# Kernel optimization log

Measured on AMD Instinct MI355X. Metric: run time of the kernel, lower is better.

The kernel has to match this reference:

```python
import jax, jax.numpy as jnp
import numpy as np

BIT_SIZE = 128  # N: bitstream length (init arg bit_size)


def setup_inputs() -> dict:
    key = jax.random.key(0)
    k1, k2 = jax.random.split(key)
    # Input bitstreams: (batch, D, N) of 0/1 bits
    inputs = jax.random.randint(k1, (64, 1024, BIT_SIZE), 0, 2, dtype=jnp.int32)
    # Learned kernel probabilities: (num_outputs, D) in [0, 1]
    kernel = jax.random.uniform(k2, (512, 1024), dtype=jnp.float32)
    return {"inputs": inputs, "kernel": kernel}


def _generate_weight_bitstreams(kernel, N):
    # Faithful vectorization of bitstream_generator_exact applied per weight:
    # exactly round(p*N) ones placed at uniformly random positions.
    p = jnp.clip(kernel, 0.0, 1.0)
    n_bits = jnp.round(p * N)  # (O, D)
    u = jax.random.uniform(jax.random.key(42), p.shape + (N,))
    # rank of each position in a random permutation
    ranks = jnp.argsort(jnp.argsort(u, axis=-1), axis=-1)  # (O, D, N)
    return (ranks < n_bits[..., None]).astype(jnp.int32)   # (O, D, N) 0/1


def reference(inputs, kernel):
    N = BIT_SIZE
    wbits = _generate_weight_bitstreams(kernel, N)  # (O, D, N)
    # AND of 0/1 bits == product; popcount-accumulate over input dim D.
    # out[b, o, t] = sum_d (w[o, d, t] & x[b, d, t])
    counts = jnp.einsum('odn,bdn->bon', wbits, inputs)  # (B, O, N) int32
    # Stochastic-computing value estimate: normalize by bitstream length.
    return counts.astype(jnp.float32) / N
```

## Files before the change

kernel.cpp:

```cpp
#include <hip/hip_runtime.h>
#include <stdint.h>

#define B_ 64
#define D_ 1024
#define O_ 512
#define N_ 128

__device__ __forceinline__ uint32_t rotl32(uint32_t x, uint32_t d) {
  return __builtin_amdgcn_alignbit(x, x, 32u - d);
}

__device__ __forceinline__ void threefry2x32(uint32_t c0, uint32_t c1,
                                             uint32_t& r0, uint32_t& r1) {
  const uint32_t ks0 = 0u;
  const uint32_t ks1 = 42u;
  const uint32_t ks2 = 0u ^ 42u ^ 0x1BD11BDAu;
  uint32_t x0 = c0 + ks0;
  uint32_t x1 = c1 + ks1;
#define RND(R) { x0 += x1; x1 = rotl32(x1, R); x1 ^= x0; }
  RND(13) RND(15) RND(26) RND(6)
  x0 += ks1; x1 += ks2 + 1u;
  RND(17) RND(29) RND(16) RND(24)
  x0 += ks2; x1 += ks0 + 2u;
  RND(13) RND(15) RND(26) RND(6)
  x0 += ks0; x1 += ks1 + 3u;
  RND(17) RND(29) RND(16) RND(24)
  x0 += ks1; x1 += ks2 + 4u;
  RND(13) RND(15) RND(26) RND(6)
  x0 += ks2; x1 += ks0 + 5u;
#undef RND
  r0 = x0; r1 = x1;
}

__device__ __forceinline__ uint32_t rand_bits(uint32_t i) {
  uint32_t a, b;
  threefry2x32(0u, i, a, b);
  return a ^ b;
}

__global__ void pack_x(const int* __restrict__ x, uint32_t* __restrict__ xp) {
  const int t   = threadIdx.x;
  const int idx = blockIdx.x;
  const int b   = idx >> 5;
  const int g   = (idx >> 2) & 7;
  const int e   = idx & 3;
  const int* src = x + ((b * D_) + (g * 128 + e * 32)) * N_ + t;
  uint32_t w = 0;
#pragma unroll
  for (int j = 0; j < 32; ++j)
    w |= (uint32_t)(src[j * N_] & 1) << j;
  xp[(((b * 8) + g) * N_ + t) * 4 + e] = w;
}

__global__ void gen_weights(const float* __restrict__ kern, uint4* __restrict__ wtmp) {
  const int lane = threadIdx.x & 63;
  const int wave = threadIdx.x >> 6;
  const int row0 = blockIdx.x * 32 + wave * 8;
  const uint32_t lane2 = (uint32_t)lane + 64u;
  const uint32_t KMASK = 0xFFFFFF80u;
  const uint32_t base_i = (uint32_t)row0 * 128u + (uint32_t)lane;

  uint32_t k0 = ((rand_bits(base_i) >> 2) & KMASK) | (uint32_t)lane;
  uint32_t k1 = ((rand_bits(base_i + 64u) >> 2) & KMASK) | lane2;
  float p0 = fminf(fmaxf(kern[row0], 0.0f), 1.0f);
  int n = (int)rintf(p0 * 128.0f);

#define PROBE_UPDATE_EXIT                                          \
      "v_cmp_lt_u32 %[q0], %[k0], %[m]\n\t"                        \
      "v_cmp_lt_u32 %[q1], %[k1], %[m]\n\t"                        \
      "s_bcnt1_i32_b64 %[c], %[q0]\n\t"                            \
      "s_bcnt1_i32_b64 %[c2], %[q1]\n\t"                           \
      "s_add_i32 %[c], %[c], %[c2]\n\t"                            \
      "s_cmp_ge_i32 %[c], %[ns]\n\t"                               \
      "s_cselect_b32 %[hi], %[m], %[hi]\n\t"                       \
      "s_cselect_b32 %[lo], %[lo], %[m]\n\t"                       \
      "s_cmp_eq_i32 %[c], %[ns]\n\t"                               \
      "s_cbranch_scc1 Ldone%=\n\t"
#define INTERP_MID                                                 \
      "s_sub_i32 %[d], %[ns], %[c]\n\t"                            \
      "s_lshl_b32 %[d], %[d], 23\n\t"                              \
      "s_add_u32 %[m], %[m], %[d]\n\t"                             \
      "s_add_u32 %[t1], %[lo], 1\n\t"                              \
      "s_add_u32 %[t2], %[hi], -1\n\t"                             \
      "s_min_u32 %[m], %[m], %[t2]\n\t"                            \
      "s_max_u32 %[m], %[m], %[t1]\n\t"

#pragma unroll
  for (int rr = 0; rr < 8; ++rr) {
    uint32_t k0n = 0, k1n = 0; int nn = 0;
    if (rr < 7) {
      const uint32_t i0 = base_i + (uint32_t)((rr + 1) * 128);
      k0n = ((rand_bits(i0) >> 2) & KMASK) | (uint32_t)lane;
      k1n = ((rand_bits(i0 + 64u) >> 2) & KMASK) | lane2;
      float p = fminf(fmaxf(kern[row0 + rr + 1], 0.0f), 1.0f);
      nn = (int)rintf(p * 128.0f);
    }

    uint64_t m0, m1;
    if (n <= 0) {
      m0 = 0ull; m1 = 0ull;
    } else if (n >= 128) {
      m0 = ~0ull; m1 = ~0ull;
    } else {
      uint64_t q0, q1;
      uint32_t lo, hi, m, c, c2, ns, d, t1, t2;
      asm volatile(
        "v_readfirstlane_b32 %[ns], %[nv]\n\t"
        "s_mov_b32 %[lo], 0\n\t"
        "s_mov_b32 %[hi], 0x40000000\n\t"
        "s_lshl_b32 %[m], %[ns], 23\n\t"
        PROBE_UPDATE_EXIT
        INTERP_MID
        PROBE_UPDATE_EXIT
        INTERP_MID
        PROBE_UPDATE_EXIT
        "Lbs%=:\n\t"
        "s_add_u32 %[m], %[lo], %[hi]\n\t"
        "s_lshr_b32 %[m], %[m], 1\n\t"
        "s_add_u32 %[t1], %[lo], 1\n\t"
        "s_max_u32 %[m], %[m], %[t1]\n\t"
        "v_cmp_lt_u32 %[q0], %[k0], %[m]\n\t"
        "v_cmp_lt_u32 %[q1], %[k1], %[m]\n\t"
        "s_bcnt1_i32_b64 %[c], %[q0]\n\t"
        "s_bcnt1_i32_b64 %[c2], %[q1]\n\t"
        "s_add_i32 %[c], %[c], %[c2]\n\t"
        "s_cmp_ge_i32 %[c], %[ns]\n\t"
        "s_cselect_b32 %[hi], %[m], %[hi]\n\t"
        "s_cselect_b32 %[lo], %[lo], %[m]\n\t"
        "s_cmp_lg_i32 %[c], %[ns]\n\t"
        "s_cbranch_scc1 Lbs%=\n\t"
        "Ldone%=:\n\t"
        : [q0] "=&s"(q0), [q1] "=&s"(q1), [lo] "=&s"(lo), [hi] "=&s"(hi),
          [m] "=&s"(m), [c] "=&s"(c), [c2] "=&s"(c2), [ns] "=&s"(ns),
          [d] "=&s"(d), [t1] "=&s"(t1), [t2] "=&s"(t2)
        : [k0] "v"(k0), [k1] "v"(k1), [nv] "v"(n)
        : "scc");
      m0 = q0; m1 = q1;
    }
    if (lane == 0) {
      wtmp[row0 + rr] = make_uint4((uint32_t)m0, (uint32_t)(m0 >> 32),
                                   (uint32_t)m1, (uint32_t)(m1 >> 32));
    }
    k0 = k0n; k1 = k1n; n = nn;
  }
#undef PROBE_UPDATE_EXIT
#undef INTERP_MID
}

__global__ void pack_w(const uint32_t* __restrict__ wtmp, uint32_t* __restrict__ wp) {
  const int t   = threadIdx.x;
  const int idx = blockIdx.x;
  const int o   = idx >> 3;
  const int g   = idx & 7;
  const int word = t >> 5, bit = t & 31;
  const uint32_t* base = wtmp + (size_t)(o * D_ + g * 128) * 4 + word;
#pragma unroll
  for (int e = 0; e < 4; ++e) {
    uint32_t w = 0;
#pragma unroll
    for (int j = 0; j < 32; ++j)
      w |= ((base[(e * 32 + j) * 4] >> bit) & 1u) << j;
    wp[(((o * 8) + g) * N_ + t) * 4 + e] = w;
  }
}

__global__ void popc_gemm(const uint4* __restrict__ wp, const uint4* __restrict__ xp,
                          float* __restrict__ out) {
  const int t     = threadIdx.x & 127;
  const int oi    = threadIdx.x >> 7;
  const int opair = blockIdx.x >> 3;
  const int btile = blockIdx.x & 7;
  const int o     = opair * 2 + oi;

  uint4 w[8];
#pragma unroll
  for (int g = 0; g < 8; ++g) w[g] = wp[(o * 8 + g) * N_ + t];

#pragma unroll
  for (int ib = 0; ib < 8; ++ib) {
    const int b = btile * 8 + ib;
    uint32_t acc = 0;
#pragma unroll
    for (int g = 0; g < 8; ++g) {
      const uint4 xv = xp[(b * 8 + g) * N_ + t];
      acc += __popc(w[g].x & xv.x);
      acc += __popc(w[g].y & xv.y);
      acc += __popc(w[g].z & xv.z);
      acc += __popc(w[g].w & xv.w);
    }
    out[((size_t)(b * O_) + o) * N_ + t] = (float)acc * (1.0f / 128.0f);
  }
}

extern "C" void kernel_launch(void* const* d_in, const int* in_sizes, int n_in,
                              void* d_out, int out_size, void* d_ws, size_t ws_size,
                              hipStream_t stream) {
  const int*   x    = (const int*)d_in[0];
  const float* kern = (const float*)d_in[1];
  float*       out  = (float*)d_out;

  char* ws = (char*)d_ws;
  uint32_t* xp   = (uint32_t*)ws;
  uint4*    wtmp = (uint4*)(ws + (1u << 20));
  uint32_t* wp   = (uint32_t*)(ws + (9u << 20));

  hipLaunchKernelGGL(pack_x,      dim3(2048),  dim3(128), 0, stream, x, xp);
  hipLaunchKernelGGL(gen_weights, dim3(16384), dim3(256), 0, stream, kern, wtmp);
  hipLaunchKernelGGL(pack_w,      dim3(4096),  dim3(128), 0, stream,
                     (const uint32_t*)wtmp, wp);
  hipLaunchKernelGGL(popc_gemm,   dim3(2048),  dim3(256), 0, stream,
                     (const uint4*)wp, (const uint4*)xp, out);
}
```

Measured before the change: 185.4 us.

## Fuse weight transpose-pack into generator via LDS and drop pack_w kernel

The weight generator now transposes its 32 row bitmasks into per-time-step packed words in shared memory and writes the packed layout directly. This removes the separate pack_w kernel, its 8 MB intermediate buffer and one launch. The packed weight layout becomes word-planar, so popc_gemm loads four strided 32-bit words instead of one uint4. One extra secant/interpolation probe step is also added to the per-row threshold search, which is meant to cut binary-search iterations.

```diff
diff --git a/kernel.cpp b/kernel.cpp
--- a/kernel.cpp
+++ b/kernel.cpp
@@ -52,7 +52,10 @@
   xp[(((b * 8) + g) * N_ + t) * 4 + e] = w;
 }
 
-__global__ void gen_weights(const float* __restrict__ kern, uint4* __restrict__ wtmp) {
+__global__ void gen_weights(const float* __restrict__ kern, uint32_t* __restrict__ wp) {
+  __shared__ uint32_t lds_m[32][4];
+  __shared__ uint32_t lds_p[2][128];
+
   const int lane = threadIdx.x & 63;
   const int wave = threadIdx.x >> 6;
   const int row0 = blockIdx.x * 32 + wave * 8;
@@ -109,6 +112,8 @@
         "s_mov_b32 %[lo], 0\n\t"
         "s_mov_b32 %[hi], 0x40000000\n\t"
         "s_lshl_b32 %[m], %[ns], 23\n\t"
+        PROBE_UPDATE_EXIT
+        INTERP_MID
         PROBE_UPDATE_EXIT
         INTERP_MID
         PROBE_UPDATE_EXIT
@@ -138,33 +143,36 @@
       m0 = q0; m1 = q1;
     }
     if (lane == 0) {
-      wtmp[row0 + rr] = make_uint4((uint32_t)m0, (uint32_t)(m0 >> 32),
-                                   (uint32_t)m1, (uint32_t)(m1 >> 32));
+      const int r = wave * 8 + rr;
+      lds_m[r][0] = (uint32_t)m0;
+      lds_m[r][1] = (uint32_t)(m0 >> 32);
+      lds_m[r][2] = (uint32_t)m1;
+      lds_m[r][3] = (uint32_t)(m1 >> 32);
     }
     k0 = k0n; k1 = k1n; n = nn;
   }
 #undef PROBE_UPDATE_EXIT
 #undef INTERP_MID
-}
-
-__global__ void pack_w(const uint32_t* __restrict__ wtmp, uint32_t* __restrict__ wp) {
-  const int t   = threadIdx.x;
-  const int idx = blockIdx.x;
-  const int o   = idx >> 3;
-  const int g   = idx & 7;
-  const int word = t >> 5, bit = t & 31;
-  const uint32_t* base = wtmp + (size_t)(o * D_ + g * 128) * 4 + word;
-#pragma unroll
-  for (int e = 0; e < 4; ++e) {
-    uint32_t w = 0;
-#pragma unroll
-    for (int j = 0; j < 32; ++j)
-      w |= ((base[(e * 32 + j) * 4] >> bit) & 1u) << j;
-    wp[(((o * 8) + g) * N_ + t) * 4 + e] = w;
-  }
-}
-
-__global__ void popc_gemm(const uint4* __restrict__ wp, const uint4* __restrict__ xp,
+
+  __syncthreads();
+  const int p  = threadIdx.x >> 7;
+  const int t  = threadIdx.x & 127;
+  const int wi = t >> 5, bit = t & 31;
+  uint32_t part = 0;
+#pragma unroll
+  for (int j = 0; j < 16; ++j)
+    part |= ((lds_m[p * 16 + j][wi] >> bit) & 1u) << (p * 16 + j);
+  lds_p[p][t] = part;
+  __syncthreads();
+  if (threadIdx.x < 128) {
+    const int o = blockIdx.x >> 5;
+    const int g = (blockIdx.x >> 2) & 7;
+    const int e = blockIdx.x & 3;
+    wp[(size_t)(((o * 8 + g) * 4 + e) * 128) + t] = lds_p[0][t] | lds_p[1][t];
+  }
+}
+
+__global__ void popc_gemm(const uint32_t* __restrict__ wp, const uint4* __restrict__ xp,
                           float* __restrict__ out) {
   const int t     = threadIdx.x & 127;
   const int oi    = threadIdx.x >> 7;
@@ -174,7 +182,13 @@
 
   uint4 w[8];
 #pragma unroll
-  for (int g = 0; g < 8; ++g) w[g] = wp[(o * 8 + g) * N_ + t];
+  for (int g = 0; g < 8; ++g) {
+    const uint32_t* wpw = wp + (size_t)((o * 8 + g) * 4) * 128 + t;
+    w[g].x = wpw[0];
+    w[g].y = wpw[128];
+    w[g].z = wpw[256];
+    w[g].w = wpw[384];
+  }
 
 #pragma unroll
   for (int ib = 0; ib < 8; ++ib) {
@@ -200,14 +214,11 @@
   float*       out  = (float*)d_out;
 
   char* ws = (char*)d_ws;
-  uint32_t* xp   = (uint32_t*)ws;
-  uint4*    wtmp = (uint4*)(ws + (1u << 20));
-  uint32_t* wp   = (uint32_t*)(ws + (9u << 20));
+  uint32_t* xp = (uint32_t*)ws;
+  uint32_t* wp = (uint32_t*)(ws + (1u << 20));
 
   hipLaunchKernelGGL(pack_x,      dim3(2048),  dim3(128), 0, stream, x, xp);
-  hipLaunchKernelGGL(gen_weights, dim3(16384), dim3(256), 0, stream, kern, wtmp);
-  hipLaunchKernelGGL(pack_w,      dim3(4096),  dim3(128), 0, stream,
-                     (const uint32_t*)wtmp, wp);
+  hipLaunchKernelGGL(gen_weights, dim3(16384), dim3(256), 0, stream, kern, wp);
   hipLaunchKernelGGL(popc_gemm,   dim3(2048),  dim3(256), 0, stream,
-                     (const uint4*)wp, (const uint4*)xp, out);
-}
+                     wp, (const uint4*)xp, out);
+}
```

Measured after the change: 176.3 us, median of 3. -4.9%, faster.
